# Kernel tuning notes

Measured on AMD Instinct MI355X. Metric: run time of the kernel, lower is better.

The kernel has to match this reference:

```python
import jax, jax.numpy as jnp
import numpy as np
from jax import lax

K = 16
EPS = 1e-5


def leaky(x):
    return jnp.where(x >= 0, x, 0.2 * x)


def group_norm(x, gamma, beta, groups):
    # x: [B, C, ...]
    B, C = x.shape[0], x.shape[1]
    xs = x.reshape(B, groups, C // groups, *x.shape[2:])
    axes = tuple(range(2, xs.ndim))
    mean = xs.mean(axis=axes, keepdims=True)
    var = xs.var(axis=axes, keepdims=True)
    xs = (xs - mean) * lax.rsqrt(var + EPS)
    x = xs.reshape(x.shape)
    pshape = (1, C) + (1,) * (x.ndim - 2)
    return x * gamma.reshape(pshape) + beta.reshape(pshape)


def knn_idx(coor_k, coor_q):
    # coor_*: [B, 3, N]; returns idx [B, Nq, K] of nearest points in coor_k
    qq = (coor_q ** 2).sum(axis=1)  # [B, Nq]
    kk = (coor_k ** 2).sum(axis=1)  # [B, Nk]
    d2 = qq[:, :, None] + kk[:, None, :] - 2.0 * jnp.einsum('bcq,bck->bqk', coor_q, coor_k)
    _, idx = lax.top_k(-d2, K)  # smallest distances
    return idx


def get_graph_feature(coor_q, x_q, coor_k, x_k):
    # x_q: [B, C, Nq], x_k: [B, C, Nk] -> [B, 2C, Nq, K]
    idx = knn_idx(coor_k, coor_q)  # [B, Nq, K]
    nbr = jax.vmap(lambda xk, ix: xk[:, ix])(x_k, idx)  # [B, C, Nq, K]
    xq = x_q[:, :, :, None]
    return jnp.concatenate([nbr - xq, jnp.broadcast_to(xq, nbr.shape)], axis=1)


def fps(xyz, npoint):
    B, N, _ = xyz.shape

    def step(carry, _):
        dist, far = carry
        centroid = jnp.take_along_axis(xyz, far[:, None, None], axis=1)  # [B,1,3]
        d = ((xyz - centroid) ** 2).sum(-1)
        dist = jnp.minimum(dist, d)
        nxt = jnp.argmax(dist, axis=-1).astype(jnp.int32)
        return (dist, nxt), far

    init = (jnp.full((B, N), 1e10, xyz.dtype), jnp.zeros((B,), jnp.int32))
    _, idx = lax.scan(step, init, None, length=npoint)
    return idx.T  # [B, npoint]


def fps_downsample(coor, x, num_group):
    fps_i = fps(jnp.transpose(coor, (0, 2, 1)), num_group)  # [B, G]
    combined = jnp.concatenate([coor, x], axis=1)  # [B, 3+C, N]
    newc = jax.vmap(lambda c, ix: c[:, ix])(combined, fps_i)  # [B, 3+C, G]
    return newc[:, :3], newc[:, 3:]


def conv1x1(w, f):
    return jnp.einsum('oc,bcqk->boqk', w, f)


def setup_inputs() -> dict:
    key = jax.random.key(0)
    ks = jax.random.split(key, 16)
    B, N = 8, 4096
    s = lambda k, sh, fan: jax.random.normal(k, sh, jnp.float32) * (1.0 / np.sqrt(fan))
    return {
        'x': jax.random.normal(ks[0], (B, 3, N), jnp.float32),
        'sample_npoints': 128,
        'w_in': s(ks[1], (8, 3), 3), 'b_in': jnp.zeros((8,), jnp.float32),
        'w1': s(ks[2], (32, 16), 16), 'g1': jnp.ones((32,), jnp.float32), 'be1': jnp.zeros((32,), jnp.float32),
        'w2': s(ks[3], (64, 64), 64), 'g2': jnp.ones((64,), jnp.float32), 'be2': jnp.zeros((64,), jnp.float32),
        'w3': s(ks[4], (64, 128), 128), 'g3': jnp.ones((64,), jnp.float32), 'be3': jnp.zeros((64,), jnp.float32),
        'w4': s(ks[5], (128, 128), 128), 'g4': jnp.ones((128,), jnp.float32), 'be4': jnp.zeros((128,), jnp.float32),
    }


def reference(x, sample_npoints, w_in, b_in, w1, g1, be1, w2, g2, be2, w3, g3, be3, w4, g4, be4):
    coor = x
    f = jnp.einsum('oc,bcn->bon', w_in, x) + b_in[None, :, None]  # input_trans

    f = get_graph_feature(coor, f, coor, f)
    f = leaky(group_norm(conv1x1(w1, f), g1, be1, 4)).max(axis=-1)
    coor_q, f_q = fps_downsample(coor, f, 512)

    f = get_graph_feature(coor_q, f_q, coor, f)
    f = leaky(group_norm(conv1x1(w2, f), g2, be2, 4)).max(axis=-1)
    coor = coor_q

    f = get_graph_feature(coor, f, coor, f)
    f = leaky(group_norm(conv1x1(w3, f), g3, be3, 4)).max(axis=-1)
    coor_q, f_q = fps_downsample(coor, f, sample_npoints)

    f = get_graph_feature(coor_q, f_q, coor, f)
    f = leaky(group_norm(conv1x1(w4, f), g4, be4, 4)).max(axis=-1)
    coor = coor_q
    return coor, f
```

## Files before the change

kernel.cpp:

```cpp
#include <hip/hip_runtime.h>
#include <cstdint>

typedef unsigned int uint;
typedef unsigned short u16;

#define DEV __device__ __forceinline__

DEV float bf2f(u16 u) { return __uint_as_float(((uint)u) << 16); }
DEV u16 f2bf(float f) {
    uint x = __float_as_uint(f);
    return (u16)((x + 0x7fffu + ((x >> 16) & 1u)) >> 16);
}

struct InPtrs { const void* p[14]; };

__global__ __launch_bounds__(256) void fused_prep(
    const void* __restrict__ xv, InPtrs ptrs, float* __restrict__ cw,
    float* __restrict__ coorT, float* __restrict__ f0,
    int* __restrict__ flag, int B, int N)
{
    __shared__ int cnt[256];
    __shared__ int sflag;
    const u16* xs = (const u16*)xv;
    int t = threadIdx.x, good = 0;
#pragma unroll
    for (int i = 0; i < 8; ++i) {
        u16 u = xs[(t * 8 + i) * 37];
        int e = (u >> 7) & 0xFF;
        good += (e >= 90 && e <= 150) ? 1 : 0;
    }
    cnt[t] = good;
    __syncthreads();
    if (t == 0) {
        int s = 0;
        for (int i = 0; i < 256; ++i) s += cnt[i];
        sflag = (s >= 1741) ? 1 : 0;
    }
    __syncthreads();
    int isbf = sflag;
    int blk = blockIdx.x;

    if (blk < 128) {
        int p = blk * 256 + t;
        int b = p / N, n = p % N;
        float c0, c1, c2;
        if (isbf) {
            const u16* x = (const u16*)xv;
            c0 = bf2f(x[(b * 3 + 0) * N + n]);
            c1 = bf2f(x[(b * 3 + 1) * N + n]);
            c2 = bf2f(x[(b * 3 + 2) * N + n]);
        } else {
            const float* x = (const float*)xv;
            c0 = x[(b * 3 + 0) * N + n];
            c1 = x[(b * 3 + 1) * N + n];
            c2 = x[(b * 3 + 2) * N + n];
        }
        coorT[p * 3 + 0] = c0; coorT[p * 3 + 1] = c1; coorT[p * 3 + 2] = c2;
        float wl[24], bl[8];
        if (isbf) {
            const u16* wr = (const u16*)ptrs.p[0];
            const u16* br = (const u16*)ptrs.p[1];
#pragma unroll
            for (int i = 0; i < 24; ++i) wl[i] = bf2f(wr[i]);
#pragma unroll
            for (int i = 0; i < 8; ++i) bl[i] = bf2f(br[i]);
        } else {
            const float* wr = (const float*)ptrs.p[0];
            const float* br = (const float*)ptrs.p[1];
#pragma unroll
            for (int i = 0; i < 24; ++i) wl[i] = wr[i];
#pragma unroll
            for (int i = 0; i < 8; ++i) bl[i] = br[i];
        }
#pragma unroll
        for (int o = 0; o < 8; ++o) {
            float v = bl[o];
            v = fmaf(wl[o * 3 + 0], c0, v);
            v = fmaf(wl[o * 3 + 1], c1, v);
            v = fmaf(wl[o * 3 + 2], c2, v);
            f0[(size_t)p * 8 + o] = v;
        }
    } else {
        const int cntb[14] = {24, 8, 512, 32, 32, 4096, 64, 64, 8192, 64, 64, 16384, 128, 128};
        int g = (blk - 128) * 256 + t;
        if (g < 29792) {
            int idx = g, bb = 0;
            while (idx >= cntb[bb]) { idx -= cntb[bb]; ++bb; }
            cw[g] = isbf ? bf2f(((const u16*)ptrs.p[bb])[idx])
                         : ((const float*)ptrs.p[bb])[idx];
        }
        if (blk == 128 && t == 0) flag[0] = isbf;
    }
}

#define KNN_INSERT(DV, IV)                                                            \
    if ((DV) < bd[15]) {                                                              \
        _Pragma("unroll")                                                             \
        for (int j = 15; j >= 1; --j) {                                               \
            bool up  = ((DV) < bd[j - 1]);                                            \
            bool chg = ((DV) < bd[j]);                                                \
            if (chg) { bd[j] = up ? bd[j - 1] : (DV); bi[j] = up ? bi[j - 1] : (IV); }\
        }                                                                             \
        if ((DV) < bd[0]) { bd[0] = (DV); bi[0] = (IV); }                             \
    }

#define FPS_DPP_STEP(CTRL)                                                           \
    {                                                                                \
        float ov = __int_as_float(__builtin_amdgcn_update_dpp(                       \
            __float_as_int(bv), __float_as_int(bv), (CTRL), 0xf, 0xf, false));       \
        int oi = __builtin_amdgcn_update_dpp(bid, bid, (CTRL), 0xf, 0xf, false);     \
        bool t = (ov > bv) || (ov == bv && oi < bid);                                \
        bv = t ? ov : bv; bid = t ? oi : bid;                                        \
    }

#define FPS_MRG_STEP(CTRL)                                                           \
    {                                                                                \
        float ov = __int_as_float(__builtin_amdgcn_update_dpp(                       \
            __float_as_int(mv), __float_as_int(mv), (CTRL), 0xf, 0xf, false));       \
        int oi = __builtin_amdgcn_update_dpp(mi, mi, (CTRL), 0xf, 0xf, false);       \
        bool t = (ov > mv) || (ov == mv && oi < mi);                                 \
        mv = t ? ov : mv; mi = t ? oi : mi;                                          \
    }

template<int N, int PTS>
__global__ __launch_bounds__(256, 2) void knn_fps_kernel(
    const float* __restrict__ xyz, int* __restrict__ idxout,
    int* __restrict__ fpsout, int npoint)
{
    __shared__ union LU {
        struct { float4 kt[256]; float2 mrg[4][64][16]; } k;
        struct { float4 sxyz[N]; float2 rp[2][4]; } f;
    } u;
    int b = blockIdx.y;
    int tid = threadIdx.x;

    if (blockIdx.x == 0) {
        int wave = tid >> 6, lane = tid & 63;
        float px[PTS], py[PTS], pz[PTS], dist[PTS];
#pragma unroll
        for (int i = 0; i < PTS; ++i) {
            int p = tid + i * 256;
            const float* pp = xyz + (size_t)(b * N + p) * 3;
            float x0 = pp[0], y0 = pp[1], z0 = pp[2];
            px[i] = x0; py[i] = y0; pz[i] = z0;
            u.f.sxyz[p] = make_float4(x0, y0, z0, 0.f);
            dist[i] = 1e10f;
        }
        __syncthreads();
        int far = 0;
        int my0 = 0, my1 = 0;
        for (int it = 0; it < npoint; ++it) {
            if (it == tid)       my0 = far;
            if (it == tid + 256) my1 = far;
            float4 cv = u.f.sxyz[far];
            float cx = cv.x, cy = cv.y, cz = cv.z;
            float bv = -1.f; int bid = 0;
#pragma unroll
            for (int i = 0; i < PTS; ++i) {
                float dx = __fsub_rn(px[i], cx);
                float dy = __fsub_rn(py[i], cy);
                float dz = __fsub_rn(pz[i], cz);
                float d = __fadd_rn(__fadd_rn(__fmul_rn(dx, dx), __fmul_rn(dy, dy)), __fmul_rn(dz, dz));
                float nd = fminf(dist[i], d);
                dist[i] = nd;
                bool t = nd > bv;
                bv = t ? nd : bv; bid = t ? (tid + i * 256) : bid;
            }
            FPS_DPP_STEP(0x0B1)
            FPS_DPP_STEP(0x04E)
            FPS_DPP_STEP(0x124)
            FPS_DPP_STEP(0x128)
            FPS_DPP_STEP(0x142)
            FPS_DPP_STEP(0x143)
            int par = it & 1;
            if (lane == 63) u.f.rp[par][wave] = make_float2(bv, __int_as_float(bid));
            __syncthreads();
            {
                float2 e = u.f.rp[par][lane & 3];
                float mv = e.x; int mi = __float_as_int(e.y);
                FPS_MRG_STEP(0x0B1)
                FPS_MRG_STEP(0x04E)
                far = __builtin_amdgcn_readfirstlane(mi);
            }
        }
        if (tid < npoint)       fpsout[b * npoint + tid] = my0;
        if (tid + 256 < npoint) fpsout[b * npoint + tid + 256] = my1;
        return;
    }

    int qloc = tid & 63;
    int wave = tid >> 6;
    int q = (blockIdx.x - 1) * 64 + qloc;

    const float* qp = xyz + (size_t)(b * N + q) * 3;
    float qx = qp[0], qy = qp[1], qz = qp[2];
    float qq = __fadd_rn(__fadd_rn(__fmul_rn(qx, qx), __fmul_rn(qy, qy)), __fmul_rn(qz, qz));
    float bd[16]; int bi[16];
#pragma unroll
    for (int j = 0; j < 16; ++j) { bd[j] = 3.4e38f; bi[j] = 0; }
    float cb_d[4]; int cb_i[4]; int cnt = 0;
#pragma unroll
    for (int s = 0; s < 4; ++s) { cb_d[s] = 3.4e38f; cb_i[s] = 0; }

    for (int t0 = 0; t0 < N; t0 += 256) {
        {
            int i = tid;
            const float* kp = xyz + (size_t)(b * N + t0 + i) * 3;
            float kx = kp[0], ky = kp[1], kz = kp[2];
            float kn = __fadd_rn(__fadd_rn(__fmul_rn(kx, kx), __fmul_rn(ky, ky)), __fmul_rn(kz, kz));
            u.k.kt[i] = make_float4(kx, ky, kz, kn);
        }
        __syncthreads();
        for (int i2 = 0; i2 < 64; ++i2) {
            int ii = wave * 64 + i2;
            float4 kv = u.k.kt[ii];
            float dot = __fadd_rn(__fadd_rn(__fmul_rn(qx, kv.x), __fmul_rn(qy, kv.y)),
                                  __fmul_rn(qz, kv.z));
            float d2 = __fsub_rn(__fadd_rn(qq, kv.w), __fmul_rn(2.0f, dot));
            bool adm = (d2 < bd[15]);
            if (adm) {
                int id = t0 + ii;
                cb_d[0] = (cnt == 0) ? d2 : cb_d[0]; cb_i[0] = (cnt == 0) ? id : cb_i[0];
                cb_d[1] = (cnt == 1) ? d2 : cb_d[1]; cb_i[1] = (cnt == 1) ? id : cb_i[1];
                cb_d[2] = (cnt == 2) ? d2 : cb_d[2]; cb_i[2] = (cnt == 2) ? id : cb_i[2];
                cb_d[3] = (cnt == 3) ? d2 : cb_d[3]; cb_i[3] = (cnt == 3) ? id : cb_i[3];
                ++cnt;
            }
            if (__any(cnt >= 4)) {
#pragma unroll
                for (int s = 0; s < 4; ++s) {
                    bool have = s < cnt;
                    float dv = have ? cb_d[s] : 3.4e38f;
                    int   iv = have ? cb_i[s] : 0;
                    KNN_INSERT(dv, iv)
                }
                cnt = 0;
            }
        }
        __syncthreads();
    }
#pragma unroll
    for (int s = 0; s < 4; ++s) {
        bool have = s < cnt;
        float dv = have ? cb_d[s] : 3.4e38f;
        int   iv = have ? cb_i[s] : 0;
        KNN_INSERT(dv, iv)
    }
#pragma unroll
    for (int j = 0; j < 16; ++j)
        u.k.mrg[wave][qloc][j] = make_float2(bd[j], __int_as_float(bi[j]));
    __syncthreads();

    if (tid < 64) {
        int qm = tid;
        int qg = (blockIdx.x - 1) * 64 + qm;
        int* op = idxout + (size_t)(b * N + qg) * 16;
        int p0 = 0, p1 = 0, p2 = 0, p3 = 0;
#pragma unroll 1
        for (int j = 0; j < 16; ++j) {
            float2 h0 = u.k.mrg[0][qm][p0], h1 = u.k.mrg[1][qm][p1];
            float2 h2 = u.k.mrg[2][qm][p2], h3 = u.k.mrg[3][qm][p3];
            float bdv = h0.x; int biv = __float_as_int(h0.y); int w_ = 0;
            int i1 = __float_as_int(h1.y);
            if (h1.x < bdv || (h1.x == bdv && i1 < biv)) { bdv = h1.x; biv = i1; w_ = 1; }
            int i2v = __float_as_int(h2.y);
            if (h2.x < bdv || (h2.x == bdv && i2v < biv)) { bdv = h2.x; biv = i2v; w_ = 2; }
            int i3 = __float_as_int(h3.y);
            if (h3.x < bdv || (h3.x == bdv && i3 < biv)) { bdv = h3.x; biv = i3; w_ = 3; }
            op[j] = biv;
            p0 += (w_ == 0); p1 += (w_ == 1); p2 += (w_ == 2); p3 += (w_ == 3);
        }
    }
}

__global__ __launch_bounds__(256) void knn_kernel(
    const float* __restrict__ qxyz, const float* __restrict__ kxyz,
    int* __restrict__ idxout, int Nq, int Nk)
{
    __shared__ float4 kt[256];
    __shared__ float2 mrg[4][64][16];
    int b = blockIdx.y;
    int qloc = threadIdx.x & 63;
    int wave = threadIdx.x >> 6;
    int q = blockIdx.x * 64 + qloc;
    bool act = q < Nq;

    float qx = 0.f, qy = 0.f, qz = 0.f, qq = 0.f;
    if (act) {
        const float* qp = qxyz + (size_t)(b * Nq + q) * 3;
        qx = qp[0]; qy = qp[1]; qz = qp[2];
        qq = __fadd_rn(__fadd_rn(__fmul_rn(qx, qx), __fmul_rn(qy, qy)), __fmul_rn(qz, qz));
    }
    float bd[16]; int bi[16];
#pragma unroll
    for (int j = 0; j < 16; ++j) { bd[j] = 3.4e38f; bi[j] = 0; }
    float cb_d[4]; int cb_i[4]; int cnt = 0;
#pragma unroll
    for (int s = 0; s < 4; ++s) { cb_d[s] = 3.4e38f; cb_i[s] = 0; }

    for (int t0 = 0; t0 < Nk; t0 += 256) {
        {
            int i = threadIdx.x;
            const float* kp = kxyz + (size_t)(b * Nk + t0 + i) * 3;
            float kx = kp[0], ky = kp[1], kz = kp[2];
            float kn = __fadd_rn(__fadd_rn(__fmul_rn(kx, kx), __fmul_rn(ky, ky)), __fmul_rn(kz, kz));
            kt[i] = make_float4(kx, ky, kz, kn);
        }
        __syncthreads();
        for (int i2 = 0; i2 < 64; ++i2) {
            int ii = wave * 64 + i2;
            float4 kv = kt[ii];
            float dot = __fadd_rn(__fadd_rn(__fmul_rn(qx, kv.x), __fmul_rn(qy, kv.y)),
                                  __fmul_rn(qz, kv.z));
            float d2 = __fsub_rn(__fadd_rn(qq, kv.w), __fmul_rn(2.0f, dot));
            bool adm = act && (d2 < bd[15]);
            if (adm) {
                int id = t0 + ii;
                cb_d[0] = (cnt == 0) ? d2 : cb_d[0]; cb_i[0] = (cnt == 0) ? id : cb_i[0];
                cb_d[1] = (cnt == 1) ? d2 : cb_d[1]; cb_i[1] = (cnt == 1) ? id : cb_i[1];
                cb_d[2] = (cnt == 2) ? d2 : cb_d[2]; cb_i[2] = (cnt == 2) ? id : cb_i[2];
                cb_d[3] = (cnt == 3) ? d2 : cb_d[3]; cb_i[3] = (cnt == 3) ? id : cb_i[3];
                ++cnt;
            }
            if (__any(cnt >= 4)) {
#pragma unroll
                for (int s = 0; s < 4; ++s) {
                    bool have = s < cnt;
                    float dv = have ? cb_d[s] : 3.4e38f;
                    int   iv = have ? cb_i[s] : 0;
                    KNN_INSERT(dv, iv)
                }
                cnt = 0;
            }
        }
        __syncthreads();
    }
#pragma unroll
    for (int s = 0; s < 4; ++s) {
        bool have = s < cnt;
        float dv = have ? cb_d[s] : 3.4e38f;
        int   iv = have ? cb_i[s] : 0;
        KNN_INSERT(dv, iv)
    }
#pragma unroll
    for (int j = 0; j < 16; ++j)
        mrg[wave][qloc][j] = make_float2(bd[j], __int_as_float(bi[j]));
    __syncthreads();

    if (threadIdx.x < 64) {
        int qm = threadIdx.x;
        int qg = blockIdx.x * 64 + qm;
        if (qg < Nq) {
            int* op = idxout + (size_t)(b * Nq + qg) * 16;
            int p0 = 0, p1 = 0, p2 = 0, p3 = 0;
#pragma unroll 1
            for (int j = 0; j < 16; ++j) {
                float2 h0 = mrg[0][qm][p0], h1 = mrg[1][qm][p1];
                float2 h2 = mrg[2][qm][p2], h3 = mrg[3][qm][p3];
                float bdv = h0.x; int biv = __float_as_int(h0.y); int w_ = 0;
                int i1 = __float_as_int(h1.y);
                if (h1.x < bdv || (h1.x == bdv && i1 < biv)) { bdv = h1.x; biv = i1; w_ = 1; }
                int i2v = __float_as_int(h2.y);
                if (h2.x < bdv || (h2.x == bdv && i2v < biv)) { bdv = h2.x; biv = i2v; w_ = 2; }
                int i3 = __float_as_int(h3.y);
                if (h3.x < bdv || (h3.x == bdv && i3 < biv)) { bdv = h3.x; biv = i3; w_ = 3; }
                op[j] = biv;
                p0 += (w_ == 0); p1 += (w_ == 1); p2 += (w_ == 2); p3 += (w_ == 3);
            }
        }
    }
}

__global__ __launch_bounds__(256) void knn_part_kernel(
    const float* __restrict__ qxyz, const float* __restrict__ kxyz,
    float2* __restrict__ pbuf, int Nq, int Nk, int nchunk)
{
    __shared__ float4 kt[256];
    __shared__ float2 mrg[4][64][16];
    int qblks = Nq / 64;
    int chunk = blockIdx.x / qblks;
    int qblk = blockIdx.x % qblks;
    int klen = Nk / nchunk;
    int klo = chunk * klen, khi = klo + klen;
    int b = blockIdx.y;
    int qloc = threadIdx.x & 63;
    int wave = threadIdx.x >> 6;
    int q = qblk * 64 + qloc;

    const float* qp = qxyz + (size_t)(b * Nq + q) * 3;
    float qx = qp[0], qy = qp[1], qz = qp[2];
    float qq = __fadd_rn(__fadd_rn(__fmul_rn(qx, qx), __fmul_rn(qy, qy)), __fmul_rn(qz, qz));
    float bd[16]; int bi[16];
#pragma unroll
    for (int j = 0; j < 16; ++j) { bd[j] = 3.4e38f; bi[j] = 0; }
    float cb_d[4]; int cb_i[4]; int cnt = 0;
#pragma unroll
    for (int s = 0; s < 4; ++s) { cb_d[s] = 3.4e38f; cb_i[s] = 0; }

    for (int t0 = klo; t0 < khi; t0 += 256) {
        {
            int i = threadIdx.x;
            const float* kp = kxyz + (size_t)(b * Nk + t0 + i) * 3;
            float kx = kp[0], ky = kp[1], kz = kp[2];
            float kn = __fadd_rn(__fadd_rn(__fmul_rn(kx, kx), __fmul_rn(ky, ky)), __fmul_rn(kz, kz));
            kt[i] = make_float4(kx, ky, kz, kn);
        }
        __syncthreads();
        for (int i2 = 0; i2 < 64; ++i2) {
            int ii = wave * 64 + i2;
            float4 kv = kt[ii];
            float dot = __fadd_rn(__fadd_rn(__fmul_rn(qx, kv.x), __fmul_rn(qy, kv.y)),
                                  __fmul_rn(qz, kv.z));
            float d2 = __fsub_rn(__fadd_rn(qq, kv.w), __fmul_rn(2.0f, dot));
            bool adm = (d2 < bd[15]);
            if (adm) {
                int id = t0 + ii;
                cb_d[0] = (cnt == 0) ? d2 : cb_d[0]; cb_i[0] = (cnt == 0) ? id : cb_i[0];
                cb_d[1] = (cnt == 1) ? d2 : cb_d[1]; cb_i[1] = (cnt == 1) ? id : cb_i[1];
                cb_d[2] = (cnt == 2) ? d2 : cb_d[2]; cb_i[2] = (cnt == 2) ? id : cb_i[2];
                cb_d[3] = (cnt == 3) ? d2 : cb_d[3]; cb_i[3] = (cnt == 3) ? id : cb_i[3];
                ++cnt;
            }
            if (__any(cnt >= 4)) {
#pragma unroll
                for (int s = 0; s < 4; ++s) {
                    bool have = s < cnt;
                    float dv = have ? cb_d[s] : 3.4e38f;
                    int   iv = have ? cb_i[s] : 0;
                    KNN_INSERT(dv, iv)
                }
                cnt = 0;
            }
        }
        __syncthreads();
    }
#pragma unroll
    for (int s = 0; s < 4; ++s) {
        bool have = s < cnt;
        float dv = have ? cb_d[s] : 3.4e38f;
        int   iv = have ? cb_i[s] : 0;
        KNN_INSERT(dv, iv)
    }
#pragma unroll
    for (int j = 0; j < 16; ++j)
        mrg[wave][qloc][j] = make_float2(bd[j], __int_as_float(bi[j]));
    __syncthreads();

    if (threadIdx.x < 64) {
        int qm = threadIdx.x;
        int qg = qblk * 64 + qm;
        float2* op = pbuf + (((size_t)(b * Nq + qg) * nchunk) + chunk) * 16;
        int p0 = 0, p1 = 0, p2 = 0, p3 = 0;
#pragma unroll 1
        for (int j = 0; j < 16; ++j) {
            float2 h0 = mrg[0][qm][p0], h1 = mrg[1][qm][p1];
            float2 h2 = mrg[2][qm][p2], h3 = mrg[3][qm][p3];
            float bdv = h0.x; int biv = __float_as_int(h0.y); int w_ = 0;
            int i1 = __float_as_int(h1.y);
            if (h1.x < bdv || (h1.x == bdv && i1 < biv)) { bdv = h1.x; biv = i1; w_ = 1; }
            int i2v = __float_as_int(h2.y);
            if (h2.x < bdv || (h2.x == bdv && i2v < biv)) { bdv = h2.x; biv = i2v; w_ = 2; }
            int i3 = __float_as_int(h3.y);
            if (h3.x < bdv || (h3.x == bdv && i3 < biv)) { bdv = h3.x; biv = i3; w_ = 3; }
            op[j] = make_float2(bdv, __int_as_float(biv));
            p0 += (w_ == 0); p1 += (w_ == 1); p2 += (w_ == 2); p3 += (w_ == 3);
        }
    }
}

__global__ void knn_merge_kernel(const float2* __restrict__ pbuf, int* __restrict__ idxout,
                                 int total)
{
    int q = blockIdx.x * 256 + threadIdx.x;
    if (q >= total) return;
    const float2* L = pbuf + (size_t)q * 64;
    int* op = idxout + (size_t)q * 16;
    int p0 = 0, p1 = 0, p2 = 0, p3 = 0;
#pragma unroll 1
    for (int j = 0; j < 16; ++j) {
        float2 h0 = L[p0], h1 = L[16 + p1], h2 = L[32 + p2], h3 = L[48 + p3];
        float bdv = h0.x; int biv = __float_as_int(h0.y); int w_ = 0;
        int i1 = __float_as_int(h1.y);
        if (h1.x < bdv || (h1.x == bdv && i1 < biv)) { bdv = h1.x; biv = i1; w_ = 1; }
        int i2v = __float_as_int(h2.y);
        if (h2.x < bdv || (h2.x == bdv && i2v < biv)) { bdv = h2.x; biv = i2v; w_ = 2; }
        int i3 = __float_as_int(h3.y);
        if (h3.x < bdv || (h3.x == bdv && i3 < biv)) { bdv = h3.x; biv = i3; w_ = 3; }
        op[j] = biv;
        p0 += (w_ == 0); p1 += (w_ == 1); p2 += (w_ == 2); p3 += (w_ == 3);
    }
}

template<int CTRL>
DEV void red5(float& v, int& i, float& x, float& y, float& z)
{
    float ov = __int_as_float(__builtin_amdgcn_update_dpp(
        __float_as_int(v), __float_as_int(v), CTRL, 0xf, 0xf, false));
    int oi = __builtin_amdgcn_update_dpp(i, i, CTRL, 0xf, 0xf, false);
    float ox = __int_as_float(__builtin_amdgcn_update_dpp(
        __float_as_int(x), __float_as_int(x), CTRL, 0xf, 0xf, false));
    float oy = __int_as_float(__builtin_amdgcn_update_dpp(
        __float_as_int(y), __float_as_int(y), CTRL, 0xf, 0xf, false));
    float oz = __int_as_float(__builtin_amdgcn_update_dpp(
        __float_as_int(z), __float_as_int(z), CTRL, 0xf, 0xf, false));
    bool t = (ov > v) || (ov == v && oi < i);
    v = t ? ov : v; i = t ? oi : i; x = t ? ox : x; y = t ? oy : y; z = t ? oz : z;
}

template<bool STORE_V>
__global__ __launch_bounds__(256) void stats3_fps_kernel(
    const float* __restrict__ fq, const float* __restrict__ fk, const int* __restrict__ idx,
    const float* __restrict__ w, float* __restrict__ partials, float* __restrict__ vbuf,
    const float* __restrict__ fxyz, int* __restrict__ fpsout, int Nq, int Nk)
{
    constexpr int K = 16, C_IN = 64, C_OUT = 64, E = 2 * C_IN, GC = C_OUT / 4;
    __shared__ alignas(16) float edge[4][K][E];
    __shared__ int nidx[4][K];
    __shared__ float gsum[4][4][2];

    int b = blockIdx.y;
    if (blockIdx.x == 0) {
        int tid = threadIdx.x;
        if (tid >= 64) return;
        constexpr int PTS = 8, NL = 512;
        float px[PTS], py[PTS], pz[PTS], dist[PTS];
#pragma unroll
        for (int i = 0; i < PTS; ++i) {
            int p = tid + i * 64;
            const float* pp = fxyz + (size_t)(b * NL + p) * 3;
            px[i] = pp[0]; py[i] = pp[1]; pz[i] = pp[2];
            dist[i] = 1e10f;
        }
        float cx = __int_as_float(__builtin_amdgcn_readlane(__float_as_int(px[0]), 0));
        float cy = __int_as_float(__builtin_amdgcn_readlane(__float_as_int(py[0]), 0));
        float cz = __int_as_float(__builtin_amdgcn_readlane(__float_as_int(pz[0]), 0));
        int curidx = 0;
        int my0 = 0, my1 = 0;
        for (int it = 0; it < 128; ++it) {
            if (it == tid)      my0 = curidx;
            if (it == tid + 64) my1 = curidx;
            float bv = -1.f; int bid = 0; float bx = 0.f, by = 0.f, bz = 0.f;
#pragma unroll
            for (int i = 0; i < PTS; ++i) {
                float dx = __fsub_rn(px[i], cx);
                float dy = __fsub_rn(py[i], cy);
                float dz = __fsub_rn(pz[i], cz);
                float d = __fadd_rn(__fadd_rn(__fmul_rn(dx, dx), __fmul_rn(dy, dy)), __fmul_rn(dz, dz));
                float nd = fminf(dist[i], d);
                dist[i] = nd;
                bool t = nd > bv;
                bv = t ? nd : bv; bid = t ? (tid + i * 64) : bid;
                bx = t ? px[i] : bx; by = t ? py[i] : by; bz = t ? pz[i] : bz;
            }
            red5<0x0B1>(bv, bid, bx, by, bz);
            red5<0x04E>(bv, bid, bx, by, bz);
            red5<0x124>(bv, bid, bx, by, bz);
            red5<0x128>(bv, bid, bx, by, bz);
            red5<0x142>(bv, bid, bx, by, bz);
            red5<0x143>(bv, bid, bx, by, bz);
            curidx = __builtin_amdgcn_readlane(bid, 63);
            cx = __int_as_float(__builtin_amdgcn_readlane(__float_as_int(bx), 63));
            cy = __int_as_float(__builtin_amdgcn_readlane(__float_as_int(by), 63));
            cz = __int_as_float(__builtin_amdgcn_readlane(__float_as_int(bz), 63));
        }
        if (tid < 128)      fpsout[b * 128 + tid] = my0;
        if (tid + 64 < 128) fpsout[b * 128 + tid + 64] = my1;
        return;
    }

    int wave = threadIdx.x >> 6, lane = threadIdx.x & 63;
    int nqc = Nq >> 2;
    int chunk = blockIdx.x - 1;
    int q = chunk * 4 + wave;

    const float* xqr = fq + (size_t)(b * Nq + q) * C_IN;
    if (lane < K) nidx[wave][lane] = idx[(size_t)(b * Nq + q) * K + lane];
    for (int t = lane; t < K * E; t += 64) {
        int k = t / E, c = t % E;
        int j = nidx[wave][k];
        float v;
        if (c < C_IN) v = fk[(size_t)(b * Nk + j) * C_IN + c] - xqr[c];
        else          v = xqr[c - C_IN];
        edge[wave][k][c] = v;
    }
    __syncthreads();

    {
        int oc = lane;
        float s = 0.f, ss = 0.f;
        float v[K];
#pragma unroll
        for (int k2 = 0; k2 < K; ++k2) v[k2] = 0.f;
        const float* wr = w + (size_t)oc * E;
        for (int c = 0; c < E; c += 4) {
            float4 wv = *reinterpret_cast<const float4*>(wr + c);
#pragma unroll
            for (int k2 = 0; k2 < K; ++k2) {
                const float4 e4 = *reinterpret_cast<const float4*>(&edge[wave][k2][c]);
                v[k2] = fmaf(wv.x, e4.x, v[k2]);
                v[k2] = fmaf(wv.y, e4.y, v[k2]);
                v[k2] = fmaf(wv.z, e4.z, v[k2]);
                v[k2] = fmaf(wv.w, e4.w, v[k2]);
            }
        }
        if (STORE_V) {
            float4* vb = (float4*)(vbuf + ((size_t)(b * Nq + q) * C_OUT + oc) * 16);
            vb[0] = make_float4(v[0], v[1], v[2], v[3]);
            vb[1] = make_float4(v[4], v[5], v[6], v[7]);
            vb[2] = make_float4(v[8], v[9], v[10], v[11]);
            vb[3] = make_float4(v[12], v[13], v[14], v[15]);
        }
#pragma unroll
        for (int k2 = 0; k2 < K; ++k2) { s += v[k2]; ss = fmaf(v[k2], v[k2], ss); }
#pragma unroll
        for (int m2 = 1; m2 < GC; m2 <<= 1) { s += __shfl_xor(s, m2); ss += __shfl_xor(ss, m2); }
        if ((oc & (GC - 1)) == 0) {
            gsum[wave][oc / GC][0] = s; gsum[wave][oc / GC][1] = ss;
        }
    }
    __syncthreads();
    if (threadIdx.x < 4) {
        int g = threadIdx.x;
        float s  = ((gsum[0][g][0] + gsum[1][g][0]) + gsum[2][g][0]) + gsum[3][g][0];
        float ss = ((gsum[0][g][1] + gsum[1][g][1]) + gsum[2][g][1]) + gsum[3][g][1];
        size_t pi = ((size_t)(b * 4 + g) * nqc + chunk) * 2;
        partials[pi] = s; partials[pi + 1] = ss;
    }
}

__global__ void gather_kernel(const float* __restrict__ coorS, const float* __restrict__ fS,
                              const int* __restrict__ fidx, float* __restrict__ coorD,
                              float* __restrict__ fD, int Ns, int M, int C)
{
    int b = blockIdx.y;
    int m = blockIdx.x * blockDim.x + threadIdx.x;
    if (m >= M) return;
    int j = fidx[b * M + m];
#pragma unroll
    for (int c = 0; c < 3; ++c)
        coorD[((size_t)b * M + m) * 3 + c] = coorS[((size_t)b * Ns + j) * 3 + c];
    for (int c = 0; c < C; ++c)
        fD[((size_t)b * M + m) * C + c] = fS[((size_t)b * Ns + j) * C + c];
}

template<int C_IN, int C_OUT, bool STORE_V>
__global__ __launch_bounds__(256) void edge_conv_stats_t(
    const float* __restrict__ fq, const float* __restrict__ fk, const int* __restrict__ idx,
    const float* __restrict__ w, float* __restrict__ partials, float* __restrict__ vbuf,
    int Nq, int Nk)
{
    constexpr int K = 16, E = 2 * C_IN, GC = C_OUT / 4;
    constexpr int ITERS = (C_OUT + 63) / 64;
    __shared__ alignas(16) float edge[4][K][E];
    __shared__ int nidx[4][K];
    __shared__ float gsum[4][4][2];

    int wave = threadIdx.x >> 6, lane = threadIdx.x & 63;
    int nqc = Nq >> 2;
    int b = blockIdx.y, chunk = blockIdx.x;
    int q = chunk * 4 + wave;

    const float* xqr = fq + (size_t)(b * Nq + q) * C_IN;
// ... 86 lines not shown
    __shared__ alignas(16) float edge[4][K][E];
    __shared__ int nidx[4][K];

    int wave = threadIdx.x >> 6, lane = threadIdx.x & 63;
    int b = blockIdx.y, chunk = blockIdx.x;
    int q = chunk * 4 + wave;

    const float* xqr = fq + (size_t)(b * Nq + q) * C_IN;
    if (lane < K) nidx[wave][lane] = idx[(size_t)(b * Nq + q) * K + lane];
    for (int t = lane; t < K * E; t += 64) {
        int k = t / E, c = t % E;
        int j = nidx[wave][k];
        float v;
        if (c < C_IN) v = fk[(size_t)(b * Nk + j) * C_IN + c] - xqr[c];
        else          v = xqr[c - C_IN];
        edge[wave][k][c] = v;
    }
    __syncthreads();

#pragma unroll
    for (int itr = 0; itr < ITERS; ++itr) {
        int oc = lane + 64 * itr;
        if (oc < C_OUT) {
            float v[K];
#pragma unroll
            for (int k2 = 0; k2 < K; ++k2) v[k2] = 0.f;
            const float* wr = w + (size_t)oc * E;
            for (int c = 0; c < E; c += 4) {
                float4 wv = *reinterpret_cast<const float4*>(wr + c);
#pragma unroll
                for (int k2 = 0; k2 < K; ++k2) {
                    const float4 e4 = *reinterpret_cast<const float4*>(&edge[wave][k2][c]);
                    v[k2] = fmaf(wv.x, e4.x, v[k2]);
                    v[k2] = fmaf(wv.y, e4.y, v[k2]);
                    v[k2] = fmaf(wv.z, e4.z, v[k2]);
                    v[k2] = fmaf(wv.w, e4.w, v[k2]);
                }
            }
            int g = oc / GC;
            float mean = stats[(b * 4 + g) * 2 + 0];
            float rstd = stats[(b * 4 + g) * 2 + 1];
            float ga = gamma[oc], be = beta[oc];
            float m = -3.4e38f;
#pragma unroll
            for (int k2 = 0; k2 < K; ++k2) {
                float y = fmaf((v[k2] - mean) * rstd, ga, be);
                y = (y >= 0.f) ? y : 0.2f * y;
                m = fmaxf(m, y);
            }
            outp[(size_t)(b * Nq + q) * C_OUT + oc] = m;
        }
    }
}

template<int C_OUT>
__global__ __launch_bounds__(256) void edge_conv_apply2(
    const float* __restrict__ vbuf, const float* __restrict__ stats,
    const float* __restrict__ gamma, const float* __restrict__ beta,
    float* __restrict__ outp, int total, int Nq)
{
    constexpr int GC = C_OUT / 4;
    int t = blockIdx.x * 256 + threadIdx.x;
    if (t >= total) return;
    int oc = t & (C_OUT - 1);
    int bq = t / C_OUT;
    int b = bq / Nq;
    int g = oc / GC;
    float mean = stats[(b * 4 + g) * 2 + 0];
    float rstd = stats[(b * 4 + g) * 2 + 1];
    float ga = gamma[oc], be = beta[oc];
    const float4* vb = (const float4*)(vbuf + (size_t)t * 16);
    float m = -3.4e38f;
#pragma unroll
    for (int j = 0; j < 4; ++j) {
        float4 v4 = vb[j];
        float y;
        y = fmaf((v4.x - mean) * rstd, ga, be); y = (y >= 0.f) ? y : 0.2f * y; m = fmaxf(m, y);
        y = fmaf((v4.y - mean) * rstd, ga, be); y = (y >= 0.f) ? y : 0.2f * y; m = fmaxf(m, y);
        y = fmaf((v4.z - mean) * rstd, ga, be); y = (y >= 0.f) ? y : 0.2f * y; m = fmaxf(m, y);
        y = fmaf((v4.w - mean) * rstd, ga, be); y = (y >= 0.f) ? y : 0.2f * y; m = fmaxf(m, y);
    }
    outp[t] = m;
}

__global__ __launch_bounds__(256) void apply2_out(
    const float* __restrict__ vbuf, const float* __restrict__ stats,
    const float* __restrict__ gamma, const float* __restrict__ beta,
    const float* __restrict__ coor2T, void* __restrict__ outv,
    const int* __restrict__ flag)
{
    int t = blockIdx.x * 256 + threadIdx.x;
    int isbf = flag[0];
    if (t < 131072) {
        int oc = t & 127;
        int bq = t >> 7;
        int b = bq >> 7;
        int q = bq & 127;
        int g = oc >> 5;
        float mean = stats[(b * 4 + g) * 2 + 0];
        float rstd = stats[(b * 4 + g) * 2 + 1];
        float ga = gamma[oc], be = beta[oc];
        const float4* vb = (const float4*)(vbuf + (size_t)t * 16);
        float m = -3.4e38f;
#pragma unroll
        for (int j = 0; j < 4; ++j) {
            float4 v4 = vb[j];
            float y;
            y = fmaf((v4.x - mean) * rstd, ga, be); y = (y >= 0.f) ? y : 0.2f * y; m = fmaxf(m, y);
            y = fmaf((v4.y - mean) * rstd, ga, be); y = (y >= 0.f) ? y : 0.2f * y; m = fmaxf(m, y);
            y = fmaf((v4.z - mean) * rstd, ga, be); y = (y >= 0.f) ? y : 0.2f * y; m = fmaxf(m, y);
            y = fmaf((v4.w - mean) * rstd, ga, be); y = (y >= 0.f) ? y : 0.2f * y; m = fmaxf(m, y);
        }
        int i = 3072 + b * 16384 + oc * 128 + q;
        if (isbf) ((u16*)outv)[i] = f2bf(m);
        else      ((float*)outv)[i] = m;
    } else if (t < 134144) {
        int i = t - 131072;
        int b = i / 384, r = i % 384;
        int c = r / 128, n = r % 128;
        float v = coor2T[((size_t)b * 128 + n) * 3 + c];
        if (isbf) ((u16*)outv)[i] = f2bf(v);
        else      ((float*)outv)[i] = v;
    }
}

__global__ void write_out_kernel(const float* __restrict__ coor2T, const float* __restrict__ f4T,
                                 void* __restrict__ outv, const int* __restrict__ flag)
{
    int i = blockIdx.x * blockDim.x + threadIdx.x;
    if (i >= 134144) return;
    float v;
    if (i < 3072) {
        int b = i / 384, r = i % 384;
        int c = r / 128, n = r % 128;
        v = coor2T[((size_t)b * 128 + n) * 3 + c];
    } else {
        int jj = i - 3072;
        int b = jj / 16384, r = jj % 16384;
        int c = r / 128, qn = r % 128;
        v = f4T[((size_t)b * 128 + qn) * 128 + c];
    }
    if (flag[0]) ((u16*)outv)[i] = f2bf(v);
    else         ((float*)outv)[i] = v;
}

extern "C" void kernel_launch(void* const* d_in, const int* in_sizes, int n_in,
                              void* d_out, int out_size, void* d_ws, size_t ws_size,
                              hipStream_t stream)
{
    (void)in_sizes; (void)n_in; (void)out_size;
    constexpr int B = 8, N = 4096, M1 = 512, M2 = 128;

    float* fbase   = (float*)d_ws;
    float* coorT   = fbase;
    float* f0T     = coorT + 98304;
    float* f1T     = f0T + 262144;
    float* f2T     = f1T + 1048576;
    float* f3T     = f2T + 262144;
    float* f4T     = f3T + 262144;
    float* coor1T  = f4T + 131072;
    float* coor2T  = coor1T + 12288;
    float* fq2T    = coor2T + 3072;
    float* fq4T    = fq2T + 131072;
    float* statsb  = fq4T + 65536;
    float* partials= statsb + 256;
    float* pb      = partials + 65536;
    float* cw      = pb + 524288;
    int* ibase = (int*)(cw + 29796);
    int* idx1 = ibase;
    int* idx2 = idx1 + 524288;
    int* idx3 = idx2 + 65536;
    int* idx4 = idx3 + 65536;
    int* fps1 = idx4 + 16384;
    int* fps2 = fps1 + 4096;
    int* flag = fps2 + 1024;

    size_t used = (size_t)((char*)(flag + 1) - (char*)d_ws);
    size_t voff = (used + 255) & ~(size_t)255;
    float* vbuf = (float*)((char*)d_ws + voff);
    bool fu1 = ws_size >= voff + (size_t)16777216 * 4;
    bool fu2 = ws_size >= voff + (size_t)4194304 * 4;
    bool fu3 = fu2;
    bool fu4 = ws_size >= voff + (size_t)2097152 * 4;

    const float* w1c  = cw + 32;
    const float* g1c  = cw + 544;
    const float* be1c = cw + 576;
    const float* w2c  = cw + 608;
    const float* g2c  = cw + 4704;
    const float* be2c = cw + 4768;
    const float* w3c  = cw + 4832;
    const float* g3c  = cw + 13024;
    const float* be3c = cw + 13088;
    const float* w4c  = cw + 13152;
    const float* g4c  = cw + 29536;
    const float* be4c = cw + 29664;

    InPtrs ptrs;
    for (int i = 0; i < 14; ++i) ptrs.p[i] = d_in[i + 2];

    fused_prep<<<245, 256, 0, stream>>>(d_in[0], ptrs, cw, coorT, f0T, flag, B, N);

    knn_fps_kernel<4096, 16><<<dim3(N / 64 + 1, B), 256, 0, stream>>>(coorT, idx1, fps1, M1);
    if (fu1) {
        edge_conv_stats_t<8, 32, true><<<dim3(N / 4, B), 256, 0, stream>>>(f0T, f0T, idx1, w1c, partials, vbuf, N, N);
        gn_finalize<<<1, 256, 0, stream>>>(partials, statsb + 0, N / 4, 1.0f / (float)(N * 16 * 8));
        edge_conv_apply2<32><<<(B * N * 32 + 255) / 256, 256, 0, stream>>>(vbuf, statsb + 0, g1c, be1c, f1T, B * N * 32, N);
    } else {
        edge_conv_stats_t<8, 32, false><<<dim3(N / 4, B), 256, 0, stream>>>(f0T, f0T, idx1, w1c, partials, vbuf, N, N);
        gn_finalize<<<1, 256, 0, stream>>>(partials, statsb + 0, N / 4, 1.0f / (float)(N * 16 * 8));
        edge_conv_apply<8, 32><<<dim3(N / 4, B), 256, 0, stream>>>(f0T, f0T, idx1, statsb + 0, w1c, g1c, be1c, f1T, N, N);
    }
    gather_kernel<<<dim3((M1 + 255) / 256, B), 256, 0, stream>>>(coorT, f1T, fps1, coor1T, fq2T, N, M1, 32);

    knn_part_kernel<<<dim3((M1 / 64) * 4, B), 256, 0, stream>>>(coor1T, coorT, (float2*)pb, M1, N, 4);
    knn_merge_kernel<<<(B * M1 + 255) / 256, 256, 0, stream>>>((const float2*)pb, idx2, B * M1);
    if (fu2) {
        edge_conv_stats_t<32, 64, true><<<dim3(M1 / 4, B), 256, 0, stream>>>(fq2T, f1T, idx2, w2c, partials, vbuf, M1, N);
        gn_finalize<<<1, 256, 0, stream>>>(partials, statsb + 64, M1 / 4, 1.0f / (float)(M1 * 16 * 16));
        edge_conv_apply2<64><<<(B * M1 * 64 + 255) / 256, 256, 0, stream>>>(vbuf, statsb + 64, g2c, be2c, f2T, B * M1 * 64, M1);
    } else {
        edge_conv_stats_t<32, 64, false><<<dim3(M1 / 4, B), 256, 0, stream>>>(fq2T, f1T, idx2, w2c, partials, vbuf, M1, N);
        gn_finalize<<<1, 256, 0, stream>>>(partials, statsb + 64, M1 / 4, 1.0f / (float)(M1 * 16 * 16));
        edge_conv_apply<32, 64><<<dim3(M1 / 4, B), 256, 0, stream>>>(fq2T, f1T, idx2, statsb + 64, w2c, g2c, be2c, f2T, M1, N);
    }

    knn_kernel<<<dim3(M1 / 64, B), 256, 0, stream>>>(coor1T, coor1T, idx3, M1, M1);
    if (fu3) {
        stats3_fps_kernel<true><<<dim3(M1 / 4 + 1, B), 256, 0, stream>>>(
            f2T, f2T, idx3, w3c, partials, vbuf, coor1T, fps2, M1, M1);
        gn_finalize<<<1, 256, 0, stream>>>(partials, statsb + 128, M1 / 4, 1.0f / (float)(M1 * 16 * 16));
        edge_conv_apply2<64><<<(B * M1 * 64 + 255) / 256, 256, 0, stream>>>(vbuf, statsb + 128, g3c, be3c, f3T, B * M1 * 64, M1);
    } else {
        stats3_fps_kernel<false><<<dim3(M1 / 4 + 1, B), 256, 0, stream>>>(
            f2T, f2T, idx3, w3c, partials, vbuf, coor1T, fps2, M1, M1);
        gn_finalize<<<1, 256, 0, stream>>>(partials, statsb + 128, M1 / 4, 1.0f / (float)(M1 * 16 * 16));
        edge_conv_apply<64, 64><<<dim3(M1 / 4, B), 256, 0, stream>>>(f2T, f2T, idx3, statsb + 128, w3c, g3c, be3c, f3T, M1, M1);
    }
    gather_kernel<<<dim3(1, B), 256, 0, stream>>>(coor1T, f3T, fps2, coor2T, fq4T, M1, M2, 64);

    knn_kernel<<<dim3((M2 + 63) / 64, B), 256, 0, stream>>>(coor2T, coor1T, idx4, M2, M1);
    if (fu4) {
        edge_conv_stats_t<64, 128, true><<<dim3(M2 / 4, B), 256, 0, stream>>>(fq4T, f3T, idx4, w4c, partials, vbuf, M2, M1);
        gn_finalize<<<1, 256, 0, stream>>>(partials, statsb + 192, M2 / 4, 1.0f / (float)(M2 * 16 * 32));
        apply2_out<<<(134144 + 255) / 256, 256, 0, stream>>>(vbuf, statsb + 192, g4c, be4c, coor2T, d_out, flag);
    } else {
        edge_conv_stats_t<64, 128, false><<<dim3(M2 / 4, B), 256, 0, stream>>>(fq4T, f3T, idx4, w4c, partials, vbuf, M2, M1);
        gn_finalize<<<1, 256, 0, stream>>>(partials, statsb + 192, M2 / 4, 1.0f / (float)(M2 * 16 * 32));
        edge_conv_apply<64, 128><<<dim3(M2 / 4, B), 256, 0, stream>>>(fq4T, f3T, idx4, statsb + 192, w4c, g4c, be4c, f4T, M2, M1);
        write_out_kernel<<<(134144 + 255) / 256, 256, 0, stream>>>(coor2T, f4T, d_out, flag);
    }
}
```

Measured before the change: 907.1 us.

## Split first FPS into resumable segments overlapped with stage-1 edge-conv kernels

The 512-step farthest-point sampling for stage 1 is split into resumable segments that save per-point min distances and the current farthest index to workspace. Segments run in an extra block of the KNN kernel, the stage-1 stats kernel and the apply kernel, and a small tail kernel finishes the rest. The goal is to hide the serial FPS latency behind the parallel edge-conv work rather than leaving it bound to one block per batch. In exchange, coordinates now come from a global float4 array instead of LDS, and the distance state makes a round trip through global memory between segments.

```diff
diff --git a/kernel.cpp b/kernel.cpp
--- a/kernel.cpp
+++ b/kernel.cpp
@@ -16,7 +16,7 @@
 
 __global__ __launch_bounds__(256) void fused_prep(
     const void* __restrict__ xv, InPtrs ptrs, float* __restrict__ cw,
-    float* __restrict__ coorT, float* __restrict__ f0,
+    float* __restrict__ coorT, float* __restrict__ coor4, float* __restrict__ f0,
     int* __restrict__ flag, int B, int N)
 {
     __shared__ int cnt[256];
@@ -56,6 +56,7 @@
             c2 = x[(b * 3 + 2) * N + n];
         }
         coorT[p * 3 + 0] = c0; coorT[p * 3 + 1] = c1; coorT[p * 3 + 2] = c2;
+        *reinterpret_cast<float4*>(coor4 + (size_t)p * 4) = make_float4(c0, c1, c2, 0.f);
         float wl[24], bl[8];
         if (isbf) {
             const u16* wr = (const u16*)ptrs.p[0];
@@ -91,6 +92,82 @@
         }
         if (blk == 128 && t == 0) flag[0] = isbf;
     }
+}
+
+#define FPS_DPP_STEP(CTRL)                                                           \
+    {                                                                                \
+        float ov = __int_as_float(__builtin_amdgcn_update_dpp(                       \
+            __float_as_int(bv), __float_as_int(bv), (CTRL), 0xf, 0xf, false));       \
+        int oi = __builtin_amdgcn_update_dpp(bid, bid, (CTRL), 0xf, 0xf, false);     \
+        bool t = (ov > bv) || (ov == bv && oi < bid);                                \
+        bv = t ? ov : bv; bid = t ? oi : bid;                                        \
+    }
+
+#define FPS_MRG_STEP(CTRL)                                                           \
+    {                                                                                \
+        float ov = __int_as_float(__builtin_amdgcn_update_dpp(                       \
+            __float_as_int(mv), __float_as_int(mv), (CTRL), 0xf, 0xf, false));       \
+        int oi = __builtin_amdgcn_update_dpp(mi, mi, (CTRL), 0xf, 0xf, false);       \
+        bool t = (ov > mv) || (ov == mv && oi < mi);                                 \
+        mv = t ? ov : mv; mi = t ? oi : mi;                                          \
+    }
+
+template<int N>
+DEV void fps_segment(const float4* __restrict__ c4, float* __restrict__ sdist,
+                     int* __restrict__ sfar, int* __restrict__ out,
+                     float2 (*rp)[4], int b, int npoint, int s0, int len)
+{
+    int tid = threadIdx.x, wave = tid >> 6, lane = tid & 63;
+    float px[16], py[16], pz[16], dist[16];
+#pragma unroll
+    for (int i = 0; i < 16; ++i) {
+        int p = tid + i * 256;
+        float4 a = c4[(size_t)b * N + p];
+        px[i] = a.x; py[i] = a.y; pz[i] = a.z;
+        dist[i] = (s0 == 0) ? 1e10f : sdist[(size_t)b * N + p];
+    }
+    int far = (s0 == 0) ? 0 : sfar[b];
+    int my0 = 0, my1 = 0;
+    int send = s0 + len;
+    for (int it = s0; it < send; ++it) {
+        if (it == tid)       my0 = far;
+        if (it == tid + 256) my1 = far;
+        float4 cv = c4[(size_t)b * N + far];
+        float cx = cv.x, cy = cv.y, cz = cv.z;
+        float bv = -1.f; int bid = 0;
+#pragma unroll
+        for (int i = 0; i < 16; ++i) {
+            float dx = __fsub_rn(px[i], cx);
+            float dy = __fsub_rn(py[i], cy);
+            float dz = __fsub_rn(pz[i], cz);
+            float d = __fadd_rn(__fadd_rn(__fmul_rn(dx, dx), __fmul_rn(dy, dy)), __fmul_rn(dz, dz));
+            float nd = fminf(dist[i], d);
+            dist[i] = nd;
+            bool t = nd > bv;
+            bv = t ? nd : bv; bid = t ? (tid + i * 256) : bid;
+        }
+        FPS_DPP_STEP(0x0B1)
+        FPS_DPP_STEP(0x04E)
+        FPS_DPP_STEP(0x124)
+        FPS_DPP_STEP(0x128)
+        FPS_DPP_STEP(0x142)
+        FPS_DPP_STEP(0x143)
+        int par = it & 1;
+        if (lane == 63) rp[par][wave] = make_float2(bv, __int_as_float(bid));
+        __syncthreads();
+        {
+            float2 e = rp[par][lane & 3];
+            float mv = e.x; int mi = __float_as_int(e.y);
+            FPS_MRG_STEP(0x0B1)
+            FPS_MRG_STEP(0x04E)
+            far = __builtin_amdgcn_readfirstlane(mi);
+        }
+    }
+    if (tid >= s0 && tid < send)                         out[b * npoint + tid] = my0;
+    if (tid + 256 >= s0 && tid + 256 < send)             out[b * npoint + tid + 256] = my1;
+#pragma unroll
+    for (int i = 0; i < 16; ++i) sdist[(size_t)b * N + tid + i * 256] = dist[i];
+    if (tid == 0) sfar[b] = far;
 }
 
 #define KNN_INSERT(DV, IV)                                                            \
@@ -104,87 +181,21 @@
         if ((DV) < bd[0]) { bd[0] = (DV); bi[0] = (IV); }                             \
     }
 
-#define FPS_DPP_STEP(CTRL)                                                           \
-    {                                                                                \
-        float ov = __int_as_float(__builtin_amdgcn_update_dpp(                       \
-            __float_as_int(bv), __float_as_int(bv), (CTRL), 0xf, 0xf, false));       \
-        int oi = __builtin_amdgcn_update_dpp(bid, bid, (CTRL), 0xf, 0xf, false);     \
-        bool t = (ov > bv) || (ov == bv && oi < bid);                                \
-        bv = t ? ov : bv; bid = t ? oi : bid;                                        \
-    }
-
-#define FPS_MRG_STEP(CTRL)                                                           \
-    {                                                                                \
-        float ov = __int_as_float(__builtin_amdgcn_update_dpp(                       \
-            __float_as_int(mv), __float_as_int(mv), (CTRL), 0xf, 0xf, false));       \
-        int oi = __builtin_amdgcn_update_dpp(mi, mi, (CTRL), 0xf, 0xf, false);       \
-        bool t = (ov > mv) || (ov == mv && oi < mi);                                 \
-        mv = t ? ov : mv; mi = t ? oi : mi;                                          \
-    }
-
-template<int N, int PTS>
+template<int N>
 __global__ __launch_bounds__(256, 2) void knn_fps_kernel(
-    const float* __restrict__ xyz, int* __restrict__ idxout,
-    int* __restrict__ fpsout, int npoint)
+    const float* __restrict__ xyz, const float4* __restrict__ c4,
+    int* __restrict__ idxout, int* __restrict__ fpsout,
+    float* __restrict__ sdist, int* __restrict__ sfar, int npoint, int s0, int len)
 {
     __shared__ union LU {
         struct { float4 kt[256]; float2 mrg[4][64][16]; } k;
-        struct { float4 sxyz[N]; float2 rp[2][4]; } f;
+        float2 rp[2][4];
     } u;
     int b = blockIdx.y;
     int tid = threadIdx.x;
 
     if (blockIdx.x == 0) {
-        int wave = tid >> 6, lane = tid & 63;
-        float px[PTS], py[PTS], pz[PTS], dist[PTS];
-#pragma unroll
-        for (int i = 0; i < PTS; ++i) {
-            int p = tid + i * 256;
-            const float* pp = xyz + (size_t)(b * N + p) * 3;
-            float x0 = pp[0], y0 = pp[1], z0 = pp[2];
-            px[i] = x0; py[i] = y0; pz[i] = z0;
-            u.f.sxyz[p] = make_float4(x0, y0, z0, 0.f);
-            dist[i] = 1e10f;
-        }
-        __syncthreads();
-        int far = 0;
-        int my0 = 0, my1 = 0;
-        for (int it = 0; it < npoint; ++it) {
-            if (it == tid)       my0 = far;
-            if (it == tid + 256) my1 = far;
-            float4 cv = u.f.sxyz[far];
-            float cx = cv.x, cy = cv.y, cz = cv.z;
-            float bv = -1.f; int bid = 0;
-#pragma unroll
-            for (int i = 0; i < PTS; ++i) {
-                float dx = __fsub_rn(px[i], cx);
-                float dy = __fsub_rn(py[i], cy);
-                float dz = __fsub_rn(pz[i], cz);
-                float d = __fadd_rn(__fadd_rn(__fmul_rn(dx, dx), __fmul_rn(dy, dy)), __fmul_rn(dz, dz));
-                float nd = fminf(dist[i], d);
-                dist[i] = nd;
-                bool t = nd > bv;
-                bv = t ? nd : bv; bid = t ? (tid + i * 256) : bid;
-            }
-            FPS_DPP_STEP(0x0B1)
-            FPS_DPP_STEP(0x04E)
-            FPS_DPP_STEP(0x124)
-            FPS_DPP_STEP(0x128)
-            FPS_DPP_STEP(0x142)
-            FPS_DPP_STEP(0x143)
-            int par = it & 1;
-            if (lane == 63) u.f.rp[par][wave] = make_float2(bv, __int_as_float(bid));
-            __syncthreads();
-            {
-                float2 e = u.f.rp[par][lane & 3];
-                float mv = e.x; int mi = __float_as_int(e.y);
-                FPS_MRG_STEP(0x0B1)
-                FPS_MRG_STEP(0x04E)
-                far = __builtin_amdgcn_readfirstlane(mi);
-            }
-        }
-        if (tid < npoint)       fpsout[b * npoint + tid] = my0;
-        if (tid + 256 < npoint) fpsout[b * npoint + tid + 256] = my1;
+        fps_segment<N>(c4, sdist, sfar, fpsout, u.rp, b, npoint, s0, len);
         return;
     }
 
@@ -271,6 +282,14 @@
             p0 += (w_ == 0); p1 += (w_ == 1); p2 += (w_ == 2); p3 += (w_ == 3);
         }
     }
+}
+
+__global__ __launch_bounds__(256, 1) void fps_tail_kernel(
+    const float4* __restrict__ c4, float* __restrict__ sdist, int* __restrict__ sfar,
+    int* __restrict__ fpsout, int npoint, int s0, int len)
+{
+    __shared__ float2 rp[2][4];
+    fps_segment<4096>(c4, sdist, sfar, fpsout, rp, blockIdx.x, npoint, s0, len);
 }
 
 __global__ __launch_bounds__(256) void knn_kernel(
@@ -508,6 +527,120 @@
 }
 
 template<bool STORE_V>
+__global__ __launch_bounds__(256) void stats1_fps_kernel(
+    const float* __restrict__ f0, const int* __restrict__ idx,
+    const float* __restrict__ w, float* __restrict__ partials, float* __restrict__ vbuf,
+    const float4* __restrict__ c4, float* __restrict__ sdist, int* __restrict__ sfar,
+    int* __restrict__ fpsout, int Nq, int s0, int len)
+{
+    constexpr int K = 16, C_IN = 8, C_OUT = 32, E = 16, GC = 8;
+    __shared__ alignas(16) float edge[4][K][E];
+    __shared__ int nidx[4][K];
+    __shared__ float gsum[4][4][2];
+    __shared__ float2 rp[2][4];
+
+    int b = blockIdx.y;
+    if (blockIdx.x == 0) {
+        fps_segment<4096>(c4, sdist, sfar, fpsout, rp, b, 512, s0, len);
+        return;
+    }
+
+    int wave = threadIdx.x >> 6, lane = threadIdx.x & 63;
+    int nqc = Nq >> 2;
+    int chunk = blockIdx.x - 1;
+    int q = chunk * 4 + wave;
+
+    const float* xqr = f0 + (size_t)(b * Nq + q) * C_IN;
+    if (lane < K) nidx[wave][lane] = idx[(size_t)(b * Nq + q) * K + lane];
+    for (int t = lane; t < K * E; t += 64) {
+        int k = t / E, c = t % E;
+        int j = nidx[wave][k];
+        float v;
+        if (c < C_IN) v = f0[(size_t)(b * Nq + j) * C_IN + c] - xqr[c];
+        else          v = xqr[c - C_IN];
+        edge[wave][k][c] = v;
+    }
+    __syncthreads();
+
+    {
+        int oc = lane;
+        float s = 0.f, ss = 0.f;
+        if (oc < C_OUT) {
+            float v[K];
+#pragma unroll
+            for (int k2 = 0; k2 < K; ++k2) v[k2] = 0.f;
+            const float* wr = w + (size_t)oc * E;
+            for (int c = 0; c < E; c += 4) {
+                float4 wv = *reinterpret_cast<const float4*>(wr + c);
+#pragma unroll
+                for (int k2 = 0; k2 < K; ++k2) {
+                    const float4 e4 = *reinterpret_cast<const float4*>(&edge[wave][k2][c]);
+                    v[k2] = fmaf(wv.x, e4.x, v[k2]);
+                    v[k2] = fmaf(wv.y, e4.y, v[k2]);
+                    v[k2] = fmaf(wv.z, e4.z, v[k2]);
+                    v[k2] = fmaf(wv.w, e4.w, v[k2]);
+                }
+            }
+            if (STORE_V) {
+                float4* vb = (float4*)(vbuf + ((size_t)(b * Nq + q) * C_OUT + oc) * 16);
+                vb[0] = make_float4(v[0], v[1], v[2], v[3]);
+                vb[1] = make_float4(v[4], v[5], v[6], v[7]);
+                vb[2] = make_float4(v[8], v[9], v[10], v[11]);
+                vb[3] = make_float4(v[12], v[13], v[14], v[15]);
+            }
+#pragma unroll
+            for (int k2 = 0; k2 < K; ++k2) { s += v[k2]; ss = fmaf(v[k2], v[k2], ss); }
+        }
+#pragma unroll
+        for (int m2 = 1; m2 < GC; m2 <<= 1) { s += __shfl_xor(s, m2); ss += __shfl_xor(ss, m2); }
+        if (oc < C_OUT && (oc & (GC - 1)) == 0) {
+            gsum[wave][oc / GC][0] = s; gsum[wave][oc / GC][1] = ss;
+        }
+    }
+    __syncthreads();
+    if (threadIdx.x < 4) {
+        int g = threadIdx.x;
+        float s  = ((gsum[0][g][0] + gsum[1][g][0]) + gsum[2][g][0]) + gsum[3][g][0];
+        float ss = ((gsum[0][g][1] + gsum[1][g][1]) + gsum[2][g][1]) + gsum[3][g][1];
+        size_t pi = ((size_t)(b * 4 + g) * nqc + chunk) * 2;
+        partials[pi] = s; partials[pi + 1] = ss;
+    }
+}
+
+__global__ __launch_bounds__(256) void apply2_seg32(
+    const float* __restrict__ vbuf, const float* __restrict__ stats,
+    const float* __restrict__ gamma, const float* __restrict__ beta,
+    float* __restrict__ outp,
+    const float4* __restrict__ c4, float* __restrict__ sdist, int* __restrict__ sfar,
+    int* __restrict__ fpsout, int s0, int len)
+{
+    __shared__ float2 rp[2][4];
+    int b = blockIdx.y;
+    if (blockIdx.x == 0) {
+        fps_segment<4096>(c4, sdist, sfar, fpsout, rp, b, 512, s0, len);
+        return;
+    }
+    int t = b * 131072 + (blockIdx.x - 1) * 256 + threadIdx.x;
+    int oc = t & 31;
+    int g = oc >> 3;
+    float mean = stats[(b * 4 + g) * 2 + 0];
+    float rstd = stats[(b * 4 + g) * 2 + 1];
+    float ga = gamma[oc], be = beta[oc];
+    const float4* vb = (const float4*)(vbuf + (size_t)t * 16);
+    float m = -3.4e38f;
+#pragma unroll
+    for (int j = 0; j < 4; ++j) {
+        float4 v4 = vb[j];
+        float y;
+        y = fmaf((v4.x - mean) * rstd, ga, be); y = (y >= 0.f) ? y : 0.2f * y; m = fmaxf(m, y);
+        y = fmaf((v4.y - mean) * rstd, ga, be); y = (y >= 0.f) ? y : 0.2f * y; m = fmaxf(m, y);
+        y = fmaf((v4.z - mean) * rstd, ga, be); y = (y >= 0.f) ? y : 0.2f * y; m = fmaxf(m, y);
+        y = fmaf((v4.w - mean) * rstd, ga, be); y = (y >= 0.f) ? y : 0.2f * y; m = fmaxf(m, y);
+    }
+    outp[t] = m;
+}
+
+template<bool STORE_V>
 __global__ __launch_bounds__(256) void stats3_fps_kernel(
     const float* __restrict__ fq, const float* __restrict__ fk, const int* __restrict__ idx,
     const float* __restrict__ w, float* __restrict__ partials, float* __restrict__ vbuf,
@@ -900,7 +1033,8 @@
     constexpr int B = 8, N = 4096, M1 = 512, M2 = 128;
 
     float* fbase   = (float*)d_ws;
-    float* coorT   = fbase;
+    float* coor4   = fbase;
+    float* coorT   = coor4 + 131072;
     float* f0T     = coorT + 98304;
     float* f1T     = f0T + 262144;
     float* f2T     = f1T + 1048576;
@@ -913,7 +1047,8 @@
     float* statsb  = fq4T + 65536;
     float* partials= statsb + 256;
     float* pb      = partials + 65536;
-    float* cw      = pb + 524288;
+    float* sdist   = pb + 524288;
+    float* cw      = sdist + 32768;
     int* ibase = (int*)(cw + 29796);
     int* idx1 = ibase;
     int* idx2 = idx1 + 524288;
@@ -922,8 +1057,9 @@
     int* fps1 = idx4 + 16384;
     int* fps2 = fps1 + 4096;
     int* flag = fps2 + 1024;
-
-    size_t used = (size_t)((char*)(flag + 1) - (char*)d_ws);
+    int* sfar = flag + 4;
+
+    size_t used = (size_t)((char*)(sfar + 8) - (char*)d_ws);
     size_t voff = (used + 255) & ~(size_t)255;
     float* vbuf = (float*)((char*)d_ws + voff);
     bool fu1 = ws_size >= voff + (size_t)16777216 * 4;
@@ -947,17 +1083,22 @@
     InPtrs ptrs;
     for (int i = 0; i < 14; ++i) ptrs.p[i] = d_in[i + 2];
 
-    fused_prep<<<245, 256, 0, stream>>>(d_in[0], ptrs, cw, coorT, f0T, flag, B, N);
-
-    knn_fps_kernel<4096, 16><<<dim3(N / 64 + 1, B), 256, 0, stream>>>(coorT, idx1, fps1, M1);
+    fused_prep<<<245, 256, 0, stream>>>(d_in[0], ptrs, cw, coorT, coor4, f0T, flag, B, N);
+
+    knn_fps_kernel<4096><<<dim3(N / 64 + 1, B), 256, 0, stream>>>(
+        coorT, (const float4*)coor4, idx1, fps1, sdist, sfar, M1, 0, 160);
     if (fu1) {
-        edge_conv_stats_t<8, 32, true><<<dim3(N / 4, B), 256, 0, stream>>>(f0T, f0T, idx1, w1c, partials, vbuf, N, N);
+        stats1_fps_kernel<true><<<dim3(N / 4 + 1, B), 256, 0, stream>>>(
+            f0T, idx1, w1c, partials, vbuf, (const float4*)coor4, sdist, sfar, fps1, N, 160, 56);
         gn_finalize<<<1, 256, 0, stream>>>(partials, statsb + 0, N / 4, 1.0f / (float)(N * 16 * 8));
-        edge_conv_apply2<32><<<(B * N * 32 + 255) / 256, 256, 0, stream>>>(vbuf, statsb + 0, g1c, be1c, f1T, B * N * 32, N);
+        apply2_seg32<<<dim3(513, B), 256, 0, stream>>>(
+            vbuf, statsb + 0, g1c, be1c, f1T, (const float4*)coor4, sdist, sfar, fps1, 216, 40);
+        fps_tail_kernel<<<B, 256, 0, stream>>>((const float4*)coor4, sdist, sfar, fps1, M1, 256, 256);
     } else {
         edge_conv_stats_t<8, 32, false><<<dim3(N / 4, B), 256, 0, stream>>>(f0T, f0T, idx1, w1c, partials, vbuf, N, N);
         gn_finalize<<<1, 256, 0, stream>>>(partials, statsb + 0, N / 4, 1.0f / (float)(N * 16 * 8));
         edge_conv_apply<8, 32><<<dim3(N / 4, B), 256, 0, stream>>>(f0T, f0T, idx1, statsb + 0, w1c, g1c, be1c, f1T, N, N);
+        fps_tail_kernel<<<B, 256, 0, stream>>>((const float4*)coor4, sdist, sfar, fps1, M1, 160, 352);
     }
     gather_kernel<<<dim3((M1 + 255) / 256, B), 256, 0, stream>>>(coorT, f1T, fps1, coor1T, fq2T, N, M1, 32);
 
```

Result: slower. 1.061 ms (+16.9%).
